# Optimization experiments

Hardware: AMD Instinct MI355X
Metric: run time of the kernel (lower is better)

The kernel has to match this reference:

```python
import jax, jax.numpy as jnp
import numpy as np

N_RF = 25   # contour integration RF extent (must be odd, 7-55)
N_CH = 96   # AlexNet conv1 feature maps


def _get_coaligned_masks(weights_type, rf_len, non_overlapping_rfs=True):
    """Faithful numpy replication of the manually-defined coalignment masks."""
    half_rf = rf_len // 2
    kernel = np.zeros((N_CH, rf_len, rf_len), dtype=np.float32)
    step = 3 if non_overlapping_rfs else 1
    pre = list(range(0, half_rf, step))
    post = list(range(half_rf + step, rf_len, step))
    kernel[10, pre, half_rf] = 1
    kernel[10, post, half_rf] = 1
    if weights_type != 'enhance':
        kernel[10, half_rf, pre] = -1
        kernel[10, half_rf, post] = -1
    kernel[5, half_rf, pre] = 1
    kernel[5, half_rf, post] = 1
    if weights_type != 'enhance':
        kernel[5, pre, half_rf] = -1
        kernel[5, post, half_rf] = -1
    kernel[54, (1, 4, 6, 9, 15, 17, 20, 23), (8, 9, 10, 11, 13, 14, 15, 16)] = 1
    kernel[64, list(range(0, half_rf, 3)), list(range(0, half_rf, 3))] = 1
    kernel[64, list(range(half_rf + 3, rf_len, 3)), list(range(half_rf + 3, rf_len, 3))] = 1
    if weights_type != 'enhance':
        kernel[64, list(range(rf_len - 1, half_rf, -3)), list(range(0, half_rf, 3))] = -1
        kernel[64, list(range(half_rf - 3, -1, -3)), list(range(half_rf + 3, rf_len, 3))] = -1
    kernel[67, :, :] = np.copy(kernel[54, :, :])
    kernel[78, (1, 3, 7, 10, 14, 17, 21, 23), (17, 16, 14, 13, 11, 10, 8, 7)] = 1
    return kernel


def setup_inputs() -> dict:
    key = jax.random.key(0)
    x = jax.random.normal(key, (128, 55, 55, N_CH), dtype=jnp.float32)  # NHWC, AlexNet conv1 output
    kernel = jnp.asarray(_get_coaligned_masks('enhance_and_suppress', N_RF))  # [ch, n, n]
    return {"x": x, "kernel": kernel}


def reference(x, kernel):
    # The per-(i,j) python loop in the original is exactly a per-channel (depthwise)
    # cross-correlation with the fixed mask kernel, SAME padding (n//2 each side),
    # followed by (identity) activation and residual add.
    ch = x.shape[-1]
    k = jnp.transpose(kernel, (1, 2, 0))[:, :, None, :]  # [n, n, 1, ch] HWIO depthwise
    lateral = jax.lax.conv_general_dilated(
        x, k,
        window_strides=(1, 1),
        padding='SAME',
        dimension_numbers=('NHWC', 'HWIO', 'NHWC'),
        feature_group_count=ch,
    )
    # activation is linear (None) -> identity
    return lateral + x
```

## Files before the change

kernel.cpp:

```cpp
#include <hip/hip_runtime.h>

#define NCH   96
#define RF    25
#define HALF  12
#define HW    55
#define PLANE (HW * HW)
#define NPIX  (128 * PLANE)
#define CAP   32
#define MAXA  4
#define NGRP  12

#define WS_META_OFF (NCH * 4 + NCH * CAP * 4 * 2)

__global__ __launch_bounds__(1024) void prep_all(
        const float* __restrict__ kern, int* __restrict__ counts,
        int* __restrict__ tap_off, float* __restrict__ tap_w,
        int* __restrict__ meta) {
    __shared__ int scnt[NCH];
    const int wave = threadIdx.x >> 6;
    const int lane = threadIdx.x & 63;
    for (int c = wave; c < NCH; c += 16) {
        const float* kc = kern + c * (RF * RF);
        int base = 0;
        for (int seg = 0; seg < RF * RF; seg += 64) {
            const int i = seg + lane;
            const float w = (i < RF * RF) ? kc[i] : 0.0f;
            const unsigned long long m = __ballot(w != 0.0f);
            const int pos = base + __popcll(m & ((1ull << lane) - 1ull));
            if (w != 0.0f && pos < CAP) {
                const int dy = i / RF, dx = i - dy * RF;
                tap_off[c * CAP + pos] = (dy << 8) | dx;
                tap_w[c * CAP + pos]   = w;
            }
            base += __popcll(m);
        }
        if (lane == 0) { counts[c] = base; scnt[c] = base; }
    }
    __syncthreads();
    if (threadIdx.x == 0) {
        int na[2] = {0, 0};
        bool fallback = false;
        for (int ch = 0; ch < NCH; ++ch) {
            if (scnt[ch] > 0) {
                if (scnt[ch] > CAP) fallback = true;
                const int h = ch / 48;
                if (na[h] < MAXA) meta[3 + h * MAXA + na[h]] = ch;
                ++na[h];
            }
        }
        if (na[0] > MAXA || na[1] > MAXA) fallback = true;
        meta[0] = fallback ? 999 : 0;
        meta[1] = na[0] < MAXA ? na[0] : MAXA;
        meta[2] = na[1] < MAXA ? na[1] : MAXA;
        for (int h = 0; h < 2; ++h)
            for (int i = na[h] < MAXA ? na[h] : MAXA; i < MAXA; ++i)
                meta[3 + h * MAXA + i] = 0;
        int ngi = 0;
        for (int h = 0; h < 2; ++h) {
            int nd = 0;
            for (int s = 0; s < 3; ++s) {
                bool act = false;
                for (int c = s * 16; c < s * 16 + 16; ++c)
                    act |= (scnt[h * 48 + c] > 0);
                if (act) { for (int g = s * 4; g < s * 4 + 4; ++g)
                               meta[38 + h * 12 + nd++] = g; }
                else     { for (int g = s * 4; g < s * 4 + 4; ++g)
                               meta[12 + ngi++] = h * NGRP + g; }
            }
            meta[36 + h] = nd;
        }
        meta[11] = ngi;
    }
}

__device__ __forceinline__ float conv_tap(const float (*shp)[56],
        const int* __restrict__ toffA, const float* __restrict__ twA,
        int cnt, int r, int col) {
    float acc = 0.0f;
    for (int t = 0; t < cnt; ++t) {
        const int off = toffA[t];
        const float w = twA[t];
        const int yy = r   + (off >> 8)  - HALF;
        const int xx = col + (off & 255) - HALF;
        const bool ok = ((unsigned)yy < (unsigned)HW) &
                        ((unsigned)xx < (unsigned)HW);
        const int yc = min(max(yy, 0), HW - 1);
        const int xc = min(max(xx, 0), HW - 1);
        const float vv = shp[yc][xc];
        acc += ok ? w * vv : 0.0f;
    }
    return acc;
}

__global__ __launch_bounds__(1024, 8) void contour_split(
        const float* __restrict__ x, const float* __restrict__ kern,
        const int* __restrict__ counts, const int* __restrict__ tap_off,
        const float* __restrict__ tap_w, const int* __restrict__ meta,
        float* __restrict__ out) {
    __shared__ float sh[MAXA][HW][56];
    __shared__ float tw[MAXA][CAP];
    __shared__ int   toff[MAXA][CAP];
    __shared__ int   tcnt[MAXA];
    __shared__ signed char c2l[48];
    __shared__ int   dgS[12];
    __shared__ int   glS[24];
    __shared__ int   ndgS, flagS;

    const int tid = threadIdx.x;
    const int b   = blockIdx.x;

    if (tid == 0) flagS = meta[0];
    __syncthreads();
    const bool fast = (flagS != 999);

    if (b >= 256) {
        if (!fast) return;
        if (tid == 0) ndgS = meta[11];
        if (tid < 24) glS[tid] = meta[12 + tid];
        __syncthreads();
        const int ngi = ndgS;
        if (ngi == 0) return;
        const int S    = 256 * 1024;
        const int gt   = (b - 256) * 1024 + tid;
        const int cols = S / ngi;
        if (gt >= cols * ngi) return;
        const int j = gt % ngi;
        const int g = glS[j];
        const float4* xs4 = (const float4*)x;
        float4*       os4 = (float4*)out;
        #pragma unroll 8
        for (int p = gt / ngi; p < NPIX; p += cols) {
            const int fi = p * 24 + g;
            os4[fi] = xs4[fi];
        }
        return;
    }

    const int n = b >> 1;
    const int h = b & 1;
    const float* xn = x   + (size_t)n * (PLANE * NCH);
    float*       on = out + (size_t)n * (PLANE * NCH);

    if (fast) {
        const int na = meta[1 + h];
        if (tid < 48) c2l[tid] = -1;
        if (tid == 0) ndgS = meta[36 + h];
        if (tid >= 128 && tid < 140) dgS[tid - 128] = meta[38 + h * 12 + (tid - 128)];
        __syncthreads();
        if (tid < na) {
            const int c = meta[3 + h * MAXA + tid];
            tcnt[tid] = counts[c];
            c2l[c - h * 48] = (signed char)tid;
        }
        if (tid >= 64 && tid < 64 + MAXA * CAP) {
            const int a = (tid - 64) / CAP, t = (tid - 64) % CAP;
            const int c = (a < na) ? meta[3 + h * MAXA + a] : h * 48;
            toff[a][t] = tap_off[c * CAP + t];
            tw[a][t]   = tap_w[c * CAP + t];
        }
        __syncthreads();

        const int ndg = ndgS;
        if (ndg == 0) return;
        const int pstep = 1024 / ndg;
        const bool on_duty = (tid < pstep * ndg);

        int g = 0, a0 = -1, a1 = -1, a2 = -1, a3 = -1, pslot = 0;
        if (on_duty) {
            const int gslot = tid % ndg;
            pslot = tid / ndg;
            g = dgS[gslot];
            const int lc = g * 4;
            a0 = c2l[lc + 0]; a1 = c2l[lc + 1];
            a2 = c2l[lc + 2]; a3 = c2l[lc + 3];
        }
        const int fbase = h * NGRP + g;
        const float4* xs = (const float4*)xn;
        float4*       os = (float4*)on;

        if (on_duty) {
            #pragma unroll 4
            for (int p = pslot; p < PLANE; p += pstep) {
                const float4 v = xs[p * 24 + fbase];
                const int r = p / HW, col = p - r * HW;
                if (a0 >= 0) sh[a0][r][col] = v.x;
                if (a1 >= 0) sh[a1][r][col] = v.y;
                if (a2 >= 0) sh[a2][r][col] = v.z;
                if (a3 >= 0) sh[a3][r][col] = v.w;
            }
        }
        __syncthreads();

        if (on_duty) {
            const int cnt0 = (a0 >= 0) ? tcnt[a0] : 0;
            const int cnt1 = (a1 >= 0) ? tcnt[a1] : 0;
            const int cnt2 = (a2 >= 0) ? tcnt[a2] : 0;
            const int cnt3 = (a3 >= 0) ? tcnt[a3] : 0;
            #pragma unroll 2
            for (int p = pslot; p < PLANE; p += pstep) {
                const int fi = p * 24 + fbase;
                float4 v = xs[fi];
                const int r = p / HW, col = p - r * HW;
                if (a0 >= 0) v.x += conv_tap(sh[a0], toff[a0], tw[a0], cnt0, r, col);
                if (a1 >= 0) v.y += conv_tap(sh[a1], toff[a1], tw[a1], cnt1, r, col);
                if (a2 >= 0) v.z += conv_tap(sh[a2], toff[a2], tw[a2], cnt2, r, col);
                if (a3 >= 0) v.w += conv_tap(sh[a3], toff[a3], tw[a3], cnt3, r, col);
                os[fi] = v;
            }
        }
    } else {
        const float4* xs = (const float4*)xn;
        float4*       os = (float4*)on;
        for (int idx = tid; idx < PLANE * NGRP; idx += 1024) {
            const int px = idx / NGRP;
            const int gg = idx - px * NGRP;
            const int r  = px / HW, col = px - r * HW;
            const int fi = px * 24 + h * NGRP + gg;
            const float4 xv = xs[fi];
            float acc[4] = {xv.x, xv.y, xv.z, xv.w};
            for (int kk = 0; kk < 4; ++kk) {
                const int c = h * 48 + gg * 4 + kk;
                const int cnt = counts[c];
                if (cnt == 0) continue;
                float aa = 0.0f;
                if (cnt <= CAP) {
                    for (int t = 0; t < cnt; ++t) {
                        const int off = tap_off[c * CAP + t];
                        const float w = tap_w[c * CAP + t];
                        const int yy = r   + (off >> 8)  - HALF;
                        const int xx = col + (off & 255) - HALF;
                        if ((unsigned)yy < (unsigned)HW &&
                            (unsigned)xx < (unsigned)HW)
                            aa += w * xn[(size_t)(yy * HW + xx) * NCH + c];
                    }
                } else {
                    for (int dy = 0; dy < RF; ++dy)
                        for (int dx = 0; dx < RF; ++dx) {
                            const float w = kern[(c * RF + dy) * RF + dx];
                            if (w == 0.0f) continue;
                            const int yy = r   + dy - HALF;
                            const int xx = col + dx - HALF;
                            if ((unsigned)yy < (unsigned)HW &&
                                (unsigned)xx < (unsigned)HW)
                                aa += w * xn[(size_t)(yy * HW + xx) * NCH + c];
                        }
                }
                acc[kk] += aa;
            }
            os[fi] = make_float4(acc[0], acc[1], acc[2], acc[3]);
        }
    }
}

extern "C" void kernel_launch(void* const* d_in, const int* in_sizes, int n_in,
                              void* d_out, int out_size, void* d_ws, size_t ws_size,
                              hipStream_t stream) {
    const float* x    = (const float*)d_in[0];
    const float* kern = (const float*)d_in[1];
    float* out = (float*)d_out;

    int*   counts  = (int*)d_ws;
    int*   tap_off = (int*)((char*)d_ws + NCH * 4);
    float* tap_w   = (float*)((char*)d_ws + NCH * 4 + NCH * CAP * 4);
    int*   meta    = (int*)((char*)d_ws + WS_META_OFF);

    prep_all<<<1, 1024, 0, stream>>>(kern, counts, tap_off, tap_w, meta);

    contour_split<<<512, 1024, 0, stream>>>(x, kern, counts, tap_off, tap_w, meta, out);
}
```

Measured before the change: 415.7 us.

## Split depthwise conv into compact lateral stage and full-tensor streaming add

```diff
diff --git a/kernel.cpp b/kernel.cpp
--- a/kernel.cpp
+++ b/kernel.cpp
@@ -10,7 +10,14 @@
 #define MAXA  4
 #define NGRP  12
 
+#define M_G2A 11
+#define M_HG  40
+
 #define WS_META_OFF (NCH * 4 + NCH * CAP * 4 * 2)
+#define WS_LAT_OFF  32768
+#define WS_NEED     (WS_LAT_OFF + 8u * NPIX * 4u)
+
+typedef float f32x4 __attribute__((ext_vector_type(4)));
 
 __global__ __launch_bounds__(1024) void prep_all(
         const float* __restrict__ kern, int* __restrict__ counts,
@@ -39,6 +46,8 @@
     __syncthreads();
     if (threadIdx.x == 0) {
         int na[2] = {0, 0};
+        int Aof[NCH];
+        int Atot = 0;
         bool fallback = false;
         for (int ch = 0; ch < NCH; ++ch) {
             if (scnt[ch] > 0) {
@@ -46,30 +55,45 @@
                 const int h = ch / 48;
                 if (na[h] < MAXA) meta[3 + h * MAXA + na[h]] = ch;
                 ++na[h];
-            }
+                Aof[ch] = Atot++;
+            } else Aof[ch] = -1;
         }
         if (na[0] > MAXA || na[1] > MAXA) fallback = true;
         meta[0] = fallback ? 999 : 0;
-        meta[1] = na[0] < MAXA ? na[0] : MAXA;
-        meta[2] = na[1] < MAXA ? na[1] : MAXA;
+        const int na0 = na[0] < MAXA ? na[0] : MAXA;
+        const int na1 = na[1] < MAXA ? na[1] : MAXA;
+        meta[1] = na0; meta[2] = na1;
         for (int h = 0; h < 2; ++h)
-            for (int i = na[h] < MAXA ? na[h] : MAXA; i < MAXA; ++i)
+            for (int i = (h ? na1 : na0); i < MAXA; ++i)
                 meta[3 + h * MAXA + i] = 0;
-        int ngi = 0;
+        for (int g = 0; g < 24; ++g) {
+            int pk = 0;
+            for (int j = 0; j < 4; ++j) {
+                const int c = g * 4 + j;
+                const int a = (scnt[c] > 0) ? Aof[c] : -1;
+                pk |= ((a < 0 ? 0xFF : a) & 0xFF) << (8 * j);
+            }
+            meta[M_G2A + g] = pk;
+        }
         for (int h = 0; h < 2; ++h) {
-            int nd = 0;
-            for (int s = 0; s < 3; ++s) {
-                bool act = false;
-                for (int c = s * 16; c < s * 16 + 16; ++c)
-                    act |= (scnt[h * 48 + c] > 0);
-                if (act) { for (int g = s * 4; g < s * 4 + 4; ++g)
-                               meta[38 + h * 12 + nd++] = g; }
-                else     { for (int g = s * 4; g < s * 4 + 4; ++g)
-                               meta[12 + ngi++] = h * NGRP + g; }
-            }
-            meta[36 + h] = nd;
-        }
-        meta[11] = ngi;
+            const int base = h ? na0 : 0;
+            int nag = 0;
+            for (int g = h * NGRP; g < h * NGRP + NGRP; ++g) {
+                int pk = 0; bool any = false;
+                for (int j = 0; j < 4; ++j) {
+                    const int c = g * 4 + j;
+                    int la = -1;
+                    if (scnt[c] > 0) { la = Aof[c] - base; any = true; }
+                    pk |= ((la < 0 ? 0xFF : la) & 0xFF) << (8 * j);
+                }
+                if (any && nag < 6) {
+                    meta[M_HG + h * 16 + 1 + 2 * nag] = g;
+                    meta[M_HG + h * 16 + 2 + 2 * nag] = pk;
+                    ++nag;
+                }
+            }
+            meta[M_HG + h * 16] = nag;
+        }
     }
 }
 
@@ -92,134 +116,112 @@
     return acc;
 }
 
-__global__ __launch_bounds__(1024, 8) void contour_split(
-        const float* __restrict__ x, const float* __restrict__ kern,
-        const int* __restrict__ counts, const int* __restrict__ tap_off,
-        const float* __restrict__ tap_w, const int* __restrict__ meta,
-        float* __restrict__ out) {
+__global__ __launch_bounds__(1024, 2) void conv_stage(
+        const float* __restrict__ x, const int* __restrict__ counts,
+        const int* __restrict__ tap_off, const float* __restrict__ tap_w,
+        const int* __restrict__ meta, float* __restrict__ latg) {
     __shared__ float sh[MAXA][HW][56];
     __shared__ float tw[MAXA][CAP];
     __shared__ int   toff[MAXA][CAP];
     __shared__ int   tcnt[MAXA];
-    __shared__ signed char c2l[48];
-    __shared__ int   dgS[12];
-    __shared__ int   glS[24];
-    __shared__ int   ndgS, flagS;
-
+    __shared__ int   gidS[6], gmapS[6];
+
+    if (meta[0] == 999) return;
     const int tid = threadIdx.x;
     const int b   = blockIdx.x;
-
-    if (tid == 0) flagS = meta[0];
+    const int n   = b >> 1;
+    const int h   = b & 1;
+    const int na  = meta[1 + h];
+    const int nag = meta[M_HG + h * 16];
+    if (na == 0 || nag == 0) return;
+
+    if (tid < 6) {
+        gidS[tid]  = meta[M_HG + h * 16 + 1 + 2 * tid];
+        gmapS[tid] = meta[M_HG + h * 16 + 2 + 2 * tid];
+    }
+    if (tid < MAXA)
+        tcnt[tid] = (tid < na) ? counts[meta[3 + h * MAXA + tid]] : 0;
+    if (tid >= 64 && tid < 64 + MAXA * CAP) {
+        const int a = (tid - 64) / CAP, t = (tid - 64) % CAP;
+        const int c = meta[3 + h * MAXA + ((a < na) ? a : 0)];
+        toff[a][t] = tap_off[c * CAP + t];
+        tw[a][t]   = tap_w[c * CAP + t];
+    }
     __syncthreads();
-    const bool fast = (flagS != 999);
-
-    if (b >= 256) {
-        if (!fast) return;
-        if (tid == 0) ndgS = meta[11];
-        if (tid < 24) glS[tid] = meta[12 + tid];
+
+    const float4* xs = (const float4*)(x + (size_t)n * (PLANE * NCH));
+
+    const int totG = PLANE * nag;
+    for (int idx = tid; idx < totG; idx += 1024) {
+        const int p    = idx / nag;
+        const int slot = idx - p * nag;
+        const int g  = gidS[slot];
+        const int mp = gmapS[slot];
+        const float4 v = xs[p * 24 + g];
+        const int r = p / HW, col = p - r * HW;
+        const int a0 = (signed char)mp,         a1 = (signed char)(mp >> 8);
+        const int a2 = (signed char)(mp >> 16), a3 = (signed char)(mp >> 24);
+        if (a0 >= 0) sh[a0][r][col] = v.x;
+        if (a1 >= 0) sh[a1][r][col] = v.y;
+        if (a2 >= 0) sh[a2][r][col] = v.z;
+        if (a3 >= 0) sh[a3][r][col] = v.w;
+    }
+    __syncthreads();
+
+    const int base = h ? meta[1] : 0;
+    const int totC = na * PLANE;
+    for (int idx = tid; idx < totC; idx += 1024) {
+        const int a = idx / PLANE, p = idx - a * PLANE;
+        const int r = p / HW, col = p - r * HW;
+        const float acc = conv_tap(sh[a], toff[a], tw[a], tcnt[a], r, col);
+        latg[(size_t)(base + a) * NPIX + n * PLANE + p] = acc;
+    }
+}
+
+__global__ __launch_bounds__(1024, 2) void stream_stage(
+        const float* __restrict__ x, const float* __restrict__ kern,
+        const int* __restrict__ counts, const int* __restrict__ tap_off,
+        const float* __restrict__ tap_w, const int* __restrict__ meta,
+        const float* __restrict__ latg, float* __restrict__ out, int force_dense) {
+    const int tid = threadIdx.x;
+    if (meta[0] != 999 && !force_dense) {
+        __shared__ int g2a[24];
+        if (tid < 24) g2a[tid] = meta[M_G2A + tid];
         __syncthreads();
-        const int ngi = ndgS;
-        if (ngi == 0) return;
-        const int S    = 256 * 1024;
-        const int gt   = (b - 256) * 1024 + tid;
-        const int cols = S / ngi;
-        if (gt >= cols * ngi) return;
-        const int j = gt % ngi;
-        const int g = glS[j];
+        if (tid >= 1008) return;
+        const int g     = tid % 24;
+        const int gslot = tid / 24;
+        const int pk = g2a[g];
+        const int a0 = (signed char)pk,         a1 = (signed char)(pk >> 8);
+        const int a2 = (signed char)(pk >> 16), a3 = (signed char)(pk >> 24);
+        const f32x4* xs = (const f32x4*)x;
+        f32x4*       os = (f32x4*)out;
+        const int stride = gridDim.x * 42;
+        #pragma unroll 4
+        for (int gp = blockIdx.x * 42 + gslot; gp < NPIX; gp += stride) {
+            const size_t fi = (size_t)gp * 24 + g;
+            f32x4 v = __builtin_nontemporal_load(&xs[fi]);
+            if (a0 >= 0) v.x += latg[(size_t)a0 * NPIX + gp];
+            if (a1 >= 0) v.y += latg[(size_t)a1 * NPIX + gp];
+            if (a2 >= 0) v.z += latg[(size_t)a2 * NPIX + gp];
+            if (a3 >= 0) v.w += latg[(size_t)a3 * NPIX + gp];
+            __builtin_nontemporal_store(v, &os[fi]);
+        }
+    } else {
         const float4* xs4 = (const float4*)x;
         float4*       os4 = (float4*)out;
-        #pragma unroll 8
-        for (int p = gt / ngi; p < NPIX; p += cols) {
-            const int fi = p * 24 + g;
-            os4[fi] = xs4[fi];
-        }
-        return;
-    }
-
-    const int n = b >> 1;
-    const int h = b & 1;
-    const float* xn = x   + (size_t)n * (PLANE * NCH);
-    float*       on = out + (size_t)n * (PLANE * NCH);
-
-    if (fast) {
-        const int na = meta[1 + h];
-        if (tid < 48) c2l[tid] = -1;
-        if (tid == 0) ndgS = meta[36 + h];
-        if (tid >= 128 && tid < 140) dgS[tid - 128] = meta[38 + h * 12 + (tid - 128)];
-        __syncthreads();
-        if (tid < na) {
-            const int c = meta[3 + h * MAXA + tid];
-            tcnt[tid] = counts[c];
-            c2l[c - h * 48] = (signed char)tid;
-        }
-        if (tid >= 64 && tid < 64 + MAXA * CAP) {
-            const int a = (tid - 64) / CAP, t = (tid - 64) % CAP;
-            const int c = (a < na) ? meta[3 + h * MAXA + a] : h * 48;
-            toff[a][t] = tap_off[c * CAP + t];
-            tw[a][t]   = tap_w[c * CAP + t];
-        }
-        __syncthreads();
-
-        const int ndg = ndgS;
-        if (ndg == 0) return;
-        const int pstep = 1024 / ndg;
-        const bool on_duty = (tid < pstep * ndg);
-
-        int g = 0, a0 = -1, a1 = -1, a2 = -1, a3 = -1, pslot = 0;
-        if (on_duty) {
-            const int gslot = tid % ndg;
-            pslot = tid / ndg;
-            g = dgS[gslot];
-            const int lc = g * 4;
-            a0 = c2l[lc + 0]; a1 = c2l[lc + 1];
-            a2 = c2l[lc + 2]; a3 = c2l[lc + 3];
-        }
-        const int fbase = h * NGRP + g;
-        const float4* xs = (const float4*)xn;
-        float4*       os = (float4*)on;
-
-        if (on_duty) {
-            #pragma unroll 4
-            for (int p = pslot; p < PLANE; p += pstep) {
-                const float4 v = xs[p * 24 + fbase];
-                const int r = p / HW, col = p - r * HW;
-                if (a0 >= 0) sh[a0][r][col] = v.x;
-                if (a1 >= 0) sh[a1][r][col] = v.y;
-                if (a2 >= 0) sh[a2][r][col] = v.z;
-                if (a3 >= 0) sh[a3][r][col] = v.w;
-            }
-        }
-        __syncthreads();
-
-        if (on_duty) {
-            const int cnt0 = (a0 >= 0) ? tcnt[a0] : 0;
-            const int cnt1 = (a1 >= 0) ? tcnt[a1] : 0;
-            const int cnt2 = (a2 >= 0) ? tcnt[a2] : 0;
-            const int cnt3 = (a3 >= 0) ? tcnt[a3] : 0;
-            #pragma unroll 2
-            for (int p = pslot; p < PLANE; p += pstep) {
-                const int fi = p * 24 + fbase;
-                float4 v = xs[fi];
-                const int r = p / HW, col = p - r * HW;
-                if (a0 >= 0) v.x += conv_tap(sh[a0], toff[a0], tw[a0], cnt0, r, col);
-                if (a1 >= 0) v.y += conv_tap(sh[a1], toff[a1], tw[a1], cnt1, r, col);
-                if (a2 >= 0) v.z += conv_tap(sh[a2], toff[a2], tw[a2], cnt2, r, col);
-                if (a3 >= 0) v.w += conv_tap(sh[a3], toff[a3], tw[a3], cnt3, r, col);
-                os[fi] = v;
-            }
-        }
-    } else {
-        const float4* xs = (const float4*)xn;
-        float4*       os = (float4*)on;
-        for (int idx = tid; idx < PLANE * NGRP; idx += 1024) {
-            const int px = idx / NGRP;
-            const int gg = idx - px * NGRP;
-            const int r  = px / HW, col = px - r * HW;
-            const int fi = px * 24 + h * NGRP + gg;
-            const float4 xv = xs[fi];
+        const long long tot = (long long)NPIX * 24;
+        for (long long ii = (long long)blockIdx.x * 1024 + tid; ii < tot;
+             ii += (long long)gridDim.x * 1024) {
+            const int gp = (int)(ii / 24);
+            const int gg = (int)(ii - (long long)gp * 24);
+            const int n  = gp / PLANE, p = gp - n * PLANE;
+            const int r  = p / HW, col = p - r * HW;
+            const float* xn = x + (size_t)n * (PLANE * NCH);
+            const float4 xv = xs4[ii];
             float acc[4] = {xv.x, xv.y, xv.z, xv.w};
             for (int kk = 0; kk < 4; ++kk) {
-                const int c = h * 48 + gg * 4 + kk;
+                const int c = gg * 4 + kk;
                 const int cnt = counts[c];
                 if (cnt == 0) continue;
                 float aa = 0.0f;
@@ -247,7 +249,7 @@
                 }
                 acc[kk] += aa;
             }
-            os[fi] = make_float4(acc[0], acc[1], acc[2], acc[3]);
+            os4[ii] = make_float4(acc[0], acc[1], acc[2], acc[3]);
         }
     }
 }
@@ -263,8 +265,13 @@
     int*   tap_off = (int*)((char*)d_ws + NCH * 4);
     float* tap_w   = (float*)((char*)d_ws + NCH * 4 + NCH * CAP * 4);
     int*   meta    = (int*)((char*)d_ws + WS_META_OFF);
+    float* latg    = (float*)((char*)d_ws + WS_LAT_OFF);
 
     prep_all<<<1, 1024, 0, stream>>>(kern, counts, tap_off, tap_w, meta);
 
-    contour_split<<<512, 1024, 0, stream>>>(x, kern, counts, tap_off, tap_w, meta, out);
-}
+    const int force_dense = (ws_size < (size_t)WS_NEED) ? 1 : 0;
+    if (!force_dense)
+        conv_stage<<<256, 1024, 0, stream>>>(x, counts, tap_off, tap_w, meta, latg);
+    stream_stage<<<2048, 1024, 0, stream>>>(x, kern, counts, tap_off, tap_w,
+                                            meta, latg, out, force_dense);
+}
```

Result: faster. 342.7 us (-17.6%).
